# Performance work log

Measured on AMD Instinct MI355X. Metric: run time of the kernel, lower is better.

The kernel has to match this reference:

```python
import jax, jax.numpy as jnp
import numpy as np

EMBED = 1024
B, S = 4, 2048


def setup_inputs() -> dict:
    key = jax.random.key(0)
    ks = jax.random.split(key, 10)
    scale = 1.0 / np.sqrt(EMBED)
    return {
        "query": jax.random.normal(ks[0], (B, S, EMBED), jnp.float32),
        "key": jax.random.normal(ks[1], (B, S, EMBED), jnp.float32),
        "value": jax.random.normal(ks[2], (B, S, EMBED), jnp.float32),
        "attn_mask": jnp.zeros((B, S, S), jnp.float32),
        "Wq": jax.random.normal(ks[3], (EMBED, EMBED), jnp.float32) * scale,
        "bq": jnp.zeros((EMBED,), jnp.float32),
        "Wk": jax.random.normal(ks[4], (EMBED, EMBED), jnp.float32) * scale,
        "bk": jnp.zeros((EMBED,), jnp.float32),
        "Wv": jax.random.normal(ks[5], (EMBED, EMBED), jnp.float32) * scale,
        "bv": jnp.zeros((EMBED,), jnp.float32),
    }


def reference(query, key, value, attn_mask, Wq, bq, Wk, bk, Wv, bv):
    # Linear projections (torch Linear: x @ W.T + b)
    q = jnp.einsum("bse,fe->bsf", query, Wq) + bq
    k = jnp.einsum("bse,fe->bsf", key, Wk) + bk
    v = jnp.einsum("bse,fe->bsf", value, Wv) + bv
    # Scaled dot-product attention; NOTE: scale is sqrt(embed_size) (full dim),
    # matching the original module exactly (num_heads is unused there).
    inv_scale = 1.0 / jnp.sqrt(jnp.asarray(q.shape[-1], q.dtype))
    qk = jnp.einsum("bqe,bke->bqk", q, k) * inv_scale + attn_mask
    attn = jax.nn.softmax(qk, axis=-1)
    # dropout_p = 0.0 (eval-mode identity)
    return jnp.einsum("bqk,bke->bqe", attn, v)
```

## Files before the change

### kernel.cpp

```cpp
#include <hip/hip_runtime.h>
#include <stdint.h>


typedef __attribute__((ext_vector_type(8))) short s8v;
typedef __attribute__((ext_vector_type(4))) float f32x4;
typedef __attribute__((ext_vector_type(4))) unsigned u32x4;

__device__ __forceinline__ unsigned short f2b(float f) {
  union { float f; unsigned u; } c; c.f = f;
  unsigned r = c.u + 0x7fffu + ((c.u >> 16) & 1u);
  return (unsigned short)(r >> 16);
}

__device__ __forceinline__ void gload_lds16(const void* gsrc, void* ldst) {
  __builtin_amdgcn_global_load_lds(
      (__attribute__((address_space(1))) unsigned int*)(uintptr_t)gsrc,
      (__attribute__((address_space(3))) unsigned int*)(unsigned)(uintptr_t)ldst,
      16, 0, 0);
}

template <int N> __device__ __forceinline__ void waitvm() {
  if constexpr (N == 4)      asm volatile("s_waitcnt vmcnt(4)" ::: "memory");
  else if constexpr (N == 3) asm volatile("s_waitcnt vmcnt(3)" ::: "memory");
  else                       asm volatile("s_waitcnt vmcnt(0)" ::: "memory");
}

struct JobF {
  const float* A; const float* B; unsigned short* C; const float* bias;
  long sAb, sBb, sCb;
  int lda, ldb, ldc, tilesN, tilesMN, bmode;
};

__global__ __launch_bounds__(512, 1) void gemmF(JobF j0, JobF j1, JobF j2,
                                                int b0, int b1) {
  constexpr int ASLOT = 256 * 64;
  constexpr int SLOT = 2 * ASLOT;
  constexpr int NT = 32;
  __shared__ __align__(16) char lds[4 * SLOT];

  const int nwg = gridDim.x;
  const int hw = blockIdx.x;
  int g = (hw & 7) * (nwg >> 3) + (hw >> 3);
  const JobF J = (g < b0) ? j0 : (g < b1) ? j1 : j2;
  g -= (g < b0) ? 0 : (g < b1) ? b0 : b1;

  const int batch = g / J.tilesMN;
  const int tt = g - batch * J.tilesMN;
  const int tm = tt / J.tilesN, tn = tt - tm * J.tilesN;
  const int brow = tm << 8, bcol = tn << 8;

  const int tid = threadIdx.x, lane = tid & 63, w = tid >> 6;
  const int wm = w >> 2, wn = w & 3;
  const int fr = lane & 15, fq = lane >> 4;

  const float* Ab = J.A + (long)batch * J.sAb;
  const float* Bb = J.B + (long)batch * J.sBb;

  const float* gsrcF[4];
  int ldsdst[4];
#pragma unroll
  for (int i = 0; i < 4; i++) {
    const int c = w + i * 8;
    const bool isA = (c < 16);
    const int cc = isA ? c : c - 16;
    const int roff = cc * 1024 + lane * 16;
    const int L = roff ^ (((roff >> 7) & 7) << 4);
    const int row = L >> 6, elem = (L & 63) >> 1;
    gsrcF[i] = (isA ? (Ab + (long)(brow + row) * J.lda)
                    : (Bb + (long)(bcol + row) * J.ldb)) + elem;
    ldsdst[i] = (isA ? 0 : ASLOT) + cc * 1024 + lane * 16;
  }

  int offA[8], offB[4];
#pragma unroll
  for (int mi = 0; mi < 8; mi++) {
    const int oa = (wm * 128 + mi * 16 + fr) * 64 + fq * 16;
    offA[mi] = oa ^ (((oa >> 7) & 7) << 4);
  }
#pragma unroll
  for (int ni = 0; ni < 4; ni++) {
    const int ob = (wn * 64 + ni * 16 + fr) * 64 + fq * 16;
    offB[ni] = ASLOT + (ob ^ (((ob >> 7) & 7) << 4));
  }

  f32x4 acc[8][4];
#pragma unroll
  for (int mi = 0; mi < 8; mi++)
#pragma unroll
    for (int ni = 0; ni < 4; ni++) acc[mi][ni] = (f32x4){0.f, 0.f, 0.f, 0.f};

  f32x4 sLo[4], sHi[4];

#define ISSUE(kt) { \
  _Pragma("unroll") \
  for (int i_ = 0; i_ < 4; i_++) { \
    const float* p_ = gsrcF[i_] + (long)(kt) * 32; \
    sLo[i_] = *(const f32x4*)p_; sHi[i_] = *(const f32x4*)(p_ + 4); } }

#define CVTWRITE(kt) { \
  char* const sb_ = lds + ((kt) & 3) * SLOT; \
  _Pragma("unroll") \
  for (int i_ = 0; i_ < 4; i_++) { \
    unsigned o0_, o1_, o2_, o3_; \
    asm("v_cvt_pk_bf16_f32 %0, %1, %2" : "=v"(o0_) : "v"(sLo[i_][0]), "v"(sLo[i_][1])); \
    asm("v_cvt_pk_bf16_f32 %0, %1, %2" : "=v"(o1_) : "v"(sLo[i_][2]), "v"(sLo[i_][3])); \
    asm("v_cvt_pk_bf16_f32 %0, %1, %2" : "=v"(o2_) : "v"(sHi[i_][0]), "v"(sHi[i_][1])); \
    asm("v_cvt_pk_bf16_f32 %0, %1, %2" : "=v"(o3_) : "v"(sHi[i_][2]), "v"(sHi[i_][3])); \
    *(u32x4*)(sb_ + ldsdst[i_]) = (u32x4){o0_, o1_, o2_, o3_}; } }

#define MFMA_BODY(t) { \
  const char* sb_ = lds + ((t) & 3) * SLOT; \
  s8v bf_[4], af_[4]; \
  _Pragma("unroll") \
  for (int ni_ = 0; ni_ < 4; ni_++) bf_[ni_] = *(const s8v*)(sb_ + offB[ni_]); \
  _Pragma("unroll") \
  for (int mi_ = 0; mi_ < 4; mi_++) af_[mi_] = *(const s8v*)(sb_ + offA[mi_]); \
  __builtin_amdgcn_s_setprio(1); \
  _Pragma("unroll") \
  for (int mi_ = 0; mi_ < 4; mi_++) \
    _Pragma("unroll") \
    for (int ni_ = 0; ni_ < 4; ni_++) \
      acc[mi_][ni_] = __builtin_amdgcn_mfma_f32_16x16x32_bf16( \
          af_[mi_], bf_[ni_], acc[mi_][ni_], 0, 0, 0); \
  __builtin_amdgcn_s_setprio(0); \
  _Pragma("unroll") \
  for (int mi_ = 0; mi_ < 4; mi_++) af_[mi_] = *(const s8v*)(sb_ + offA[4 + mi_]); \
  __builtin_amdgcn_s_setprio(1); \
  _Pragma("unroll") \
  for (int mi_ = 0; mi_ < 4; mi_++) \
    _Pragma("unroll") \
    for (int ni_ = 0; ni_ < 4; ni_++) \
      acc[4 + mi_][ni_] = __builtin_amdgcn_mfma_f32_16x16x32_bf16( \
          af_[mi_], bf_[ni_], acc[4 + mi_][ni_], 0, 0, 0); \
  __builtin_amdgcn_s_setprio(0); }

#define ENDBAR() { \
  asm volatile("s_waitcnt lgkmcnt(0)" ::: "memory"); \
  __builtin_amdgcn_s_barrier(); }

  ISSUE(0);
  CVTWRITE(0);
  ISSUE(1);
  ENDBAR();

  for (int t = 0; t < NT; ++t) {
    MFMA_BODY(t);
    if (t + 1 < NT) {
      CVTWRITE(t + 1);
      if (t + 2 < NT) ISSUE(t + 2);
      ENDBAR();
    }
  }

  const long cB = (long)batch * J.sCb;
#pragma unroll
  for (int mi = 0; mi < 8; mi++) {
    const int rbase = brow + wm * 128 + mi * 16 + fq * 4;
#pragma unroll
    for (int ni = 0; ni < 4; ni++) {
      const int col = bcol + wn * 64 + ni * 16 + fr;
      const float bc = (J.bmode == 1) ? J.bias[col] : 0.f;
#pragma unroll
      for (int r = 0; r < 4; r++) {
        const int row = rbase + r;
        float v = acc[mi][ni][r] + ((J.bmode == 2) ? J.bias[row] : bc);
        J.C[cB + (long)row * J.ldc + col] = f2b(v);
      }
    }
  }
#undef ISSUE
#undef CVTWRITE
#undef MFMA_BODY
#undef ENDBAR
}

struct Job {
  const unsigned short* A; const unsigned short* B; void* C;
  const float* bias; const float* mask; float* sRow;
  long sAb, sBb, sCb, sMb;
  int lda, ldb, ldc, ldM;
  int K, tilesN, tilesMN;
  float scale; int bmode;
};

template <int NFRAG, int MODE>
__global__ __launch_bounds__(512, 2) void gemmJ(Job j0, Job j1, Job j2,
                                                int b0, int b1) {
  constexpr int BN = NFRAG * 64;
  constexpr int ASLOT = 256 * 64;
  constexpr int BSLOT = BN * 64;
  constexpr int SLOT = ASLOT + BSLOT;
  constexpr int CH = SLOT / 1024;
  constexpr int GPW = CH / 8;
  static_assert(4 * SLOT <= 160 * 1024, "LDS budget");
  __shared__ __align__(16) char lds[4 * SLOT];

  const int nwg = gridDim.x;
  const int hw = blockIdx.x;
  int g = (hw & 7) * (nwg >> 3) + (hw >> 3);
  const Job J = (g < b0) ? j0 : (g < b1) ? j1 : j2;
  g -= (g < b0) ? 0 : (g < b1) ? b0 : b1;

  const int batch = g / J.tilesMN;
  const int tt = g - batch * J.tilesMN;
  const int tm = tt / J.tilesN, tn = tt - tm * J.tilesN;
  const int brow = tm << 8, bcol = tn * BN;

  const int tid = threadIdx.x;
  const int lane = tid & 63, w = tid >> 6;
  const int wm = w >> 2, wn = w & 3;
  const int fr = lane & 15, fq = lane >> 4;

  const unsigned short* Ab = J.A + (long)batch * J.sAb;
  const unsigned short* Bb = J.B + (long)batch * J.sBb;

  const unsigned short* gsrc[GPW];
  int ldsdst[GPW];
#pragma unroll
  for (int i = 0; i < GPW; i++) {
    const int c = w + i * 8;
    const bool isA = (c < 16);
    const int cc = isA ? c : c - 16;
    const int roff = cc * 1024 + lane * 16;
    const int L = roff ^ (((roff >> 7) & 7) << 4);
    const int row = L >> 6, colb = L & 63;
    gsrc[i] = (isA ? (Ab + (long)(brow + row) * J.lda)
                   : (Bb + (long)(bcol + row) * J.ldb)) + (colb >> 1);
    ldsdst[i] = (isA ? 0 : ASLOT) + cc * 1024;
  }

  int offA[8], offB[NFRAG];
#pragma unroll
  for (int mi = 0; mi < 8; mi++) {
    const int oa = (wm * 128 + mi * 16 + fr) * 64 + fq * 16;
    offA[mi] = oa ^ (((oa >> 7) & 7) << 4);
  }
#pragma unroll
  for (int ni = 0; ni < NFRAG; ni++) {
    const int ob = (wn * (NFRAG * 16) + ni * 16 + fr) * 64 + fq * 16;
    offB[ni] = ASLOT + (ob ^ (((ob >> 7) & 7) << 4));
  }

  f32x4 acc[8][NFRAG];
#pragma unroll
  for (int mi = 0; mi < 8; mi++)
#pragma unroll
    for (int ni = 0; ni < NFRAG; ni++) acc[mi][ni] = (f32x4){0.f, 0.f, 0.f, 0.f};

  const int NT = J.K >> 5;

#define STAGE(kt) { \
  char* const sb_ = lds + ((kt) & 3) * SLOT; \
  _Pragma("unroll") \
  for (int i_ = 0; i_ < GPW; i_++) \
    gload_lds16(gsrc[i_] + (long)(kt) * 32, sb_ + ldsdst[i_]); }

  STAGE(0);
  STAGE(1);
  waitvm<GPW>();
  __builtin_amdgcn_s_barrier();

  for (int t = 0; t < NT; ++t) {
    const char* sb = lds + (t & 3) * SLOT;
    if (t + 2 < NT) STAGE(t + 2);

    s8v bf[NFRAG], af[4];
#pragma unroll
    for (int ni = 0; ni < NFRAG; ni++) bf[ni] = *(const s8v*)(sb + offB[ni]);
#pragma unroll
    for (int mi = 0; mi < 4; mi++) af[mi] = *(const s8v*)(sb + offA[mi]);
    __builtin_amdgcn_s_setprio(1);
#pragma unroll
    for (int mi = 0; mi < 4; mi++)
#pragma unroll
      for (int ni = 0; ni < NFRAG; ni++)
        acc[mi][ni] = __builtin_amdgcn_mfma_f32_16x16x32_bf16(
            af[mi], bf[ni], acc[mi][ni], 0, 0, 0);
    __builtin_amdgcn_s_setprio(0);
#pragma unroll
    for (int mi = 0; mi < 4; mi++) af[mi] = *(const s8v*)(sb + offA[4 + mi]);
    __builtin_amdgcn_s_setprio(1);
#pragma unroll
    for (int mi = 0; mi < 4; mi++)
#pragma unroll
      for (int ni = 0; ni < NFRAG; ni++)
        acc[4 + mi][ni] = __builtin_amdgcn_mfma_f32_16x16x32_bf16(
            af[mi], bf[ni], acc[4 + mi][ni], 0, 0, 0);
    __builtin_amdgcn_s_setprio(0);

    if (t + 1 < NT) {
      if (t + 2 < NT) waitvm<GPW>();
      else            waitvm<0>();
      __builtin_amdgcn_s_barrier();
    }
  }

  unsigned short* Cb = (unsigned short*)J.C;
  float* Cf = (float*)J.C;
  const long cB = (long)batch * J.sCb;
  const float* maskB = (MODE == 1) ? (J.mask + (long)batch * J.sMb) : nullptr;
  float* sB = J.sRow + batch * 2048;

#pragma unroll
  for (int mi = 0; mi < 8; mi++) {
    const int rbase = brow + wm * 128 + mi * 16 + fq * 4;

    if constexpr (MODE == 1) {
      if (J.bmode != 0) {
#pragma unroll
        for (int ni = 0; ni < NFRAG; ni++) {
          const int col = bcol + wn * (NFRAG * 16) + ni * 16 + fr;
          const float bc = (J.bmode == 1) ? J.bias[col] : 0.f;
#pragma unroll
          for (int r = 0; r < 4; r++) {
            const int row = rbase + r;
            float v = acc[mi][ni][r] + ((J.bmode == 2) ? J.bias[row] : bc);
            Cb[cB + (long)row * J.ldc + col] = f2b(v);
          }
        }
      } else {
        float rs[4] = {0.f, 0.f, 0.f, 0.f};
#pragma unroll
        for (int ni = 0; ni < NFRAG; ni++) {
          const int col = bcol + wn * (NFRAG * 16) + ni * 16 + fr;
#pragma unroll
          for (int r = 0; r < 4; r++) {
            const int row = rbase + r;
            float v = acc[mi][ni][r] * J.scale + maskB[(long)row * J.ldM + col];
            v = __expf(v);
            Cb[cB + (long)row * J.ldc + col] = f2b(v);
            rs[r] += v;
          }
        }
#pragma unroll
        for (int off = 1; off < 16; off <<= 1) {
#pragma unroll
          for (int r = 0; r < 4; r++) rs[r] += __shfl_xor(rs[r], off, 64);
        }
        if (fr == 0) {
#pragma unroll
          for (int r = 0; r < 4; r++) atomicAdd(&sB[rbase + r], rs[r]);
        }
      }
    } else {
      float inv[4];
#pragma unroll
      for (int r = 0; r < 4; r++) inv[r] = 1.0f / sB[rbase + r];
#pragma unroll
      for (int ni = 0; ni < NFRAG; ni++) {
        const int col = bcol + wn * (NFRAG * 16) + ni * 16 + fr;
#pragma unroll
        for (int r = 0; r < 4; r++) {
          const int row = rbase + r;
          Cf[cB + (long)row * J.ldc + col] = acc[mi][ni][r] * inv[r];
        }
      }
    }
  }
#undef STAGE
}

__global__ __launch_bounds__(256) void cvtW(
    const float* v, unsigned short* xv,
    const float* Wv, unsigned short* Wvb, float* sz) {
  int bid = blockIdx.x;
  if (bid >= 896) {
    for (int i = (bid - 896) * 256 + threadIdx.x; i < 8192; i += 2048)
      sz[i] = 0.f;
    return;
  }
  const float* src; unsigned short* dst; long n8; int lb, nb;
  if (bid < 768) { src = v;  dst = xv;  n8 = 1048576; lb = bid;       nb = 768; }
  else           { src = Wv; dst = Wvb; n8 = 131072;  lb = bid - 768; nb = 128; }
  const long stride = (long)nb * 256;
  for (long i = (long)lb * 256 + threadIdx.x; i < n8; i += stride) {
    const float* p = src + i * 8;
    f32x4 va = *(const f32x4*)p;
    f32x4 vb = *(const f32x4*)(p + 4);
    s8v o;
    o[0] = (short)f2b(va[0]); o[1] = (short)f2b(va[1]);
    o[2] = (short)f2b(va[2]); o[3] = (short)f2b(va[3]);
    o[4] = (short)f2b(vb[0]); o[5] = (short)f2b(vb[1]);
    o[6] = (short)f2b(vb[2]); o[7] = (short)f2b(vb[3]);
    *(s8v*)(dst + i * 8) = o;
  }
}

extern "C" void kernel_launch(void* const* d_in, const int* in_sizes, int n_in,
                              void* d_out, int out_size, void* d_ws, size_t ws_size,
                              hipStream_t stream) {
  const float* q    = (const float*)d_in[0];
  const float* k    = (const float*)d_in[1];
  const float* v    = (const float*)d_in[2];
  const float* mask = (const float*)d_in[3];
  const float* Wq   = (const float*)d_in[4];
  const float* bq   = (const float*)d_in[5];
  const float* Wk   = (const float*)d_in[6];
  const float* bk   = (const float*)d_in[7];
  const float* Wv   = (const float*)d_in[8];
  const float* bv   = (const float*)d_in[9];
  float* out = (float*)d_out;

  const size_t MB = 1ull << 20;
  if (ws_size < 134 * MB) return;
  char* ws = (char*)d_ws;
  unsigned short* qb  = (unsigned short*)(ws + 0 * MB);
  unsigned short* kb  = (unsigned short*)(ws + 16 * MB);
  unsigned short* vT  = (unsigned short*)(ws + 32 * MB);
  float*          sRw = (float*)(ws + 48 * MB);
  unsigned short* Sb  = (unsigned short*)(ws + 80 * MB);
  unsigned short* xv  = (unsigned short*)(ws + 112 * MB);
  unsigned short* Wvb = (unsigned short*)(ws + 132 * MB);

  cvtW<<<904, 256, 0, stream>>>(v, xv, Wv, Wvb, sRw);

  JobF fq = { q, Wq, qb, bq, 0, 0, 0, 1024, 1024, 1024, 4, 128, 1 };
  JobF fk = { k, Wk, kb, bk, 0, 0, 0, 1024, 1024, 1024, 4, 128, 1 };
  gemmF<<<256, 512, 0, stream>>>(fq, fk, fk, 128, 256);

  Job js = { qb, kb, (void*)Sb, nullptr, mask, sRw,
             2048L * 1024, 2048L * 1024, 2048L * 2048, 2048L * 2048,
             1024, 1024, 2048, 2048, 1024, 8, 64, 0.03125f, 0 };
  Job jv = { Wvb, xv, (void*)vT, bv, nullptr, sRw,
             0, 2048L * 1024, 1024L * 2048, 0,
             1024, 1024, 2048, 0, 1024, 8, 32, 1.0f, 2 };
  gemmJ<4, 1><<<384, 512, 0, stream>>>(js, js, jv, 256, 256);

  Job jp = { Sb, vT, (void*)out, nullptr, nullptr, sRw,
             2048L * 2048, 1024L * 2048, 2048L * 1024, 0,
             2048, 2048, 1024, 0, 2048, 8, 64, 1.0f, 0 };
  gemmJ<2, 2><<<256, 512, 0, stream>>>(jp, jp, jp, 256, 256);
}
```

Before: 216.1 us.

## Replace QK^T/V-projection GEMM with 1024-thread 16-wave kernel using 256x256 tiles

Adds gemmJ16, a 1024-thread (16-wave) workgroup kernel computing 256x256 output tiles with a 4-slot LDS ring and a prefetch distance of two stages. It replaces the 512-thread gemmJ<4,1> launch for the fused QK^T+exp and V-projection jobs, and the MODE==1 epilogue is removed from the templated kernel. The aim is more waves per tile to hide latency and a smaller per-wave accumulator footprint. The trade-off is one workgroup per CU and a shallower prefetch pipeline.

```diff
diff --git a/kernel.cpp b/kernel.cpp
--- a/kernel.cpp
+++ b/kernel.cpp
@@ -22,6 +22,7 @@
 template <int N> __device__ __forceinline__ void waitvm() {
   if constexpr (N == 4)      asm volatile("s_waitcnt vmcnt(4)" ::: "memory");
   else if constexpr (N == 3) asm volatile("s_waitcnt vmcnt(3)" ::: "memory");
+  else if constexpr (N == 2) asm volatile("s_waitcnt vmcnt(2)" ::: "memory");
   else                       asm volatile("s_waitcnt vmcnt(0)" ::: "memory");
 }
 
@@ -183,6 +184,150 @@
   float scale; int bmode;
 };
 
+__global__ __launch_bounds__(1024, 1) void gemmJ16(Job j0, Job j1, Job j2,
+                                                   int b0, int b1) {
+  constexpr int ASLOT = 256 * 64;
+  constexpr int SLOT = 2 * ASLOT;
+  __shared__ __align__(16) char lds[4 * SLOT];
+
+  const int nwg = gridDim.x;
+  const int hw = blockIdx.x;
+  int g = (hw & 7) * (nwg >> 3) + (hw >> 3);
+  const Job J = (g < b0) ? j0 : (g < b1) ? j1 : j2;
+  g -= (g < b0) ? 0 : (g < b1) ? b0 : b1;
+
+  const int batch = g / J.tilesMN;
+  const int tt = g - batch * J.tilesMN;
+  const int tm = tt / J.tilesN, tn = tt - tm * J.tilesN;
+  const int brow = tm << 8, bcol = tn << 8;
+
+  const int tid = threadIdx.x;
+  const int lane = tid & 63, w = tid >> 6;
+  const int wm = w >> 2, wn = w & 3;
+  const int fr = lane & 15, fq = lane >> 4;
+
+  const unsigned short* Ab = J.A + (long)batch * J.sAb;
+  const unsigned short* Bb = J.B + (long)batch * J.sBb;
+
+  const unsigned short* gsrc[2];
+  int ldsdst[2];
+#pragma unroll
+  for (int i = 0; i < 2; i++) {
+    const int c = w + i * 16;
+    const bool isA = (c < 16);
+    const int cc = isA ? c : c - 16;
+    const int roff = cc * 1024 + lane * 16;
+    const int L = roff ^ (((roff >> 7) & 7) << 4);
+    const int row = L >> 6, colb = L & 63;
+    gsrc[i] = (isA ? (Ab + (long)(brow + row) * J.lda)
+                   : (Bb + (long)(bcol + row) * J.ldb)) + (colb >> 1);
+    ldsdst[i] = (isA ? 0 : ASLOT) + cc * 1024;
+  }
+
+  int offA[4], offB[4];
+#pragma unroll
+  for (int mi = 0; mi < 4; mi++) {
+    const int oa = (wm * 64 + mi * 16 + fr) * 64 + fq * 16;
+    offA[mi] = oa ^ (((oa >> 7) & 7) << 4);
+  }
+#pragma unroll
+  for (int ni = 0; ni < 4; ni++) {
+    const int ob = (wn * 64 + ni * 16 + fr) * 64 + fq * 16;
+    offB[ni] = ASLOT + (ob ^ (((ob >> 7) & 7) << 4));
+  }
+
+  f32x4 acc[4][4];
+#pragma unroll
+  for (int mi = 0; mi < 4; mi++)
+#pragma unroll
+    for (int ni = 0; ni < 4; ni++) acc[mi][ni] = (f32x4){0.f, 0.f, 0.f, 0.f};
+
+  const int NT = J.K >> 5;
+
+#define STAGE16(kt) { \
+  char* const sb_ = lds + ((kt) & 3) * SLOT; \
+  gload_lds16(gsrc[0] + (long)(kt) * 32, sb_ + ldsdst[0]); \
+  gload_lds16(gsrc[1] + (long)(kt) * 32, sb_ + ldsdst[1]); }
+
+  STAGE16(0);
+  STAGE16(1);
+  waitvm<2>();
+  __builtin_amdgcn_s_barrier();
+
+  for (int t = 0; t < NT; ++t) {
+    const char* sb = lds + (t & 3) * SLOT;
+    if (t + 2 < NT) STAGE16(t + 2);
+
+    s8v bf[4], af[4];
+#pragma unroll
+    for (int ni = 0; ni < 4; ni++) bf[ni] = *(const s8v*)(sb + offB[ni]);
+#pragma unroll
+    for (int mi = 0; mi < 4; mi++) af[mi] = *(const s8v*)(sb + offA[mi]);
+    __builtin_amdgcn_s_setprio(1);
+#pragma unroll
+    for (int mi = 0; mi < 4; mi++)
+#pragma unroll
+      for (int ni = 0; ni < 4; ni++)
+        acc[mi][ni] = __builtin_amdgcn_mfma_f32_16x16x32_bf16(
+            af[mi], bf[ni], acc[mi][ni], 0, 0, 0);
+    __builtin_amdgcn_s_setprio(0);
+
+    if (t + 1 < NT) {
+      if (t + 2 < NT) waitvm<2>();
+      else            waitvm<0>();
+      __builtin_amdgcn_s_barrier();
+    }
+  }
+
+  unsigned short* Cb = (unsigned short*)J.C;
+  const long cB = (long)batch * J.sCb;
+  const float* maskB = J.mask + (long)batch * J.sMb;
+  float* sB = J.sRow + batch * 2048;
+
+#pragma unroll
+  for (int mi = 0; mi < 4; mi++) {
+    const int rbase = brow + wm * 64 + mi * 16 + fq * 4;
+
+    if (J.bmode != 0) {
+#pragma unroll
+      for (int ni = 0; ni < 4; ni++) {
+        const int col = bcol + wn * 64 + ni * 16 + fr;
+        const float bc = (J.bmode == 1) ? J.bias[col] : 0.f;
+#pragma unroll
+        for (int r = 0; r < 4; r++) {
+          const int row = rbase + r;
+          float v = acc[mi][ni][r] + ((J.bmode == 2) ? J.bias[row] : bc);
+          Cb[cB + (long)row * J.ldc + col] = f2b(v);
+        }
+      }
+    } else {
+      float rs[4] = {0.f, 0.f, 0.f, 0.f};
+#pragma unroll
+      for (int ni = 0; ni < 4; ni++) {
+        const int col = bcol + wn * 64 + ni * 16 + fr;
+#pragma unroll
+        for (int r = 0; r < 4; r++) {
+          const int row = rbase + r;
+          float v = acc[mi][ni][r] * J.scale + maskB[(long)row * J.ldM + col];
+          v = __expf(v);
+          Cb[cB + (long)row * J.ldc + col] = f2b(v);
+          rs[r] += v;
+        }
+      }
+#pragma unroll
+      for (int off = 1; off < 16; off <<= 1) {
+#pragma unroll
+        for (int r = 0; r < 4; r++) rs[r] += __shfl_xor(rs[r], off, 64);
+      }
+      if (fr == 0) {
+#pragma unroll
+        for (int r = 0; r < 4; r++) atomicAdd(&sB[rbase + r], rs[r]);
+      }
+    }
+  }
+#undef STAGE16
+}
+
 template <int NFRAG, int MODE>
 __global__ __launch_bounds__(512, 2) void gemmJ(Job j0, Job j1, Job j2,
                                                 int b0, int b1) {
@@ -192,7 +337,6 @@
   constexpr int SLOT = ASLOT + BSLOT;
   constexpr int CH = SLOT / 1024;
   constexpr int GPW = CH / 8;
-  static_assert(4 * SLOT <= 160 * 1024, "LDS budget");
   __shared__ __align__(16) char lds[4 * SLOT];
 
   const int nwg = gridDim.x;
@@ -295,65 +439,23 @@
     }
   }
 
-  unsigned short* Cb = (unsigned short*)J.C;
   float* Cf = (float*)J.C;
   const long cB = (long)batch * J.sCb;
-  const float* maskB = (MODE == 1) ? (J.mask + (long)batch * J.sMb) : nullptr;
   float* sB = J.sRow + batch * 2048;
 
 #pragma unroll
   for (int mi = 0; mi < 8; mi++) {
     const int rbase = brow + wm * 128 + mi * 16 + fq * 4;
-
-    if constexpr (MODE == 1) {
-      if (J.bmode != 0) {
-#pragma unroll
-        for (int ni = 0; ni < NFRAG; ni++) {
-          const int col = bcol + wn * (NFRAG * 16) + ni * 16 + fr;
-          const float bc = (J.bmode == 1) ? J.bias[col] : 0.f;
-#pragma unroll
-          for (int r = 0; r < 4; r++) {
-            const int row = rbase + r;
-            float v = acc[mi][ni][r] + ((J.bmode == 2) ? J.bias[row] : bc);
-            Cb[cB + (long)row * J.ldc + col] = f2b(v);
-          }
-        }
-      } else {
-        float rs[4] = {0.f, 0.f, 0.f, 0.f};
-#pragma unroll
-        for (int ni = 0; ni < NFRAG; ni++) {
-          const int col = bcol + wn * (NFRAG * 16) + ni * 16 + fr;
-#pragma unroll
-          for (int r = 0; r < 4; r++) {
-            const int row = rbase + r;
-            float v = acc[mi][ni][r] * J.scale + maskB[(long)row * J.ldM + col];
-            v = __expf(v);
-            Cb[cB + (long)row * J.ldc + col] = f2b(v);
-            rs[r] += v;
-          }
-        }
-#pragma unroll
-        for (int off = 1; off < 16; off <<= 1) {
-#pragma unroll
-          for (int r = 0; r < 4; r++) rs[r] += __shfl_xor(rs[r], off, 64);
-        }
-        if (fr == 0) {
-#pragma unroll
-          for (int r = 0; r < 4; r++) atomicAdd(&sB[rbase + r], rs[r]);
-        }
-      }
-    } else {
-      float inv[4];
-#pragma unroll
-      for (int r = 0; r < 4; r++) inv[r] = 1.0f / sB[rbase + r];
-#pragma unroll
-      for (int ni = 0; ni < NFRAG; ni++) {
-        const int col = bcol + wn * (NFRAG * 16) + ni * 16 + fr;
-#pragma unroll
-        for (int r = 0; r < 4; r++) {
-          const int row = rbase + r;
-          Cf[cB + (long)row * J.ldc + col] = acc[mi][ni][r] * inv[r];
-        }
+    float inv[4];
+#pragma unroll
+    for (int r = 0; r < 4; r++) inv[r] = 1.0f / sB[rbase + r];
+#pragma unroll
+    for (int ni = 0; ni < NFRAG; ni++) {
+      const int col = bcol + wn * (NFRAG * 16) + ni * 16 + fr;
+#pragma unroll
+      for (int r = 0; r < 4; r++) {
+        const int row = rbase + r;
+        Cf[cB + (long)row * J.ldc + col] = acc[mi][ni][r] * inv[r];
       }
     }
   }
@@ -421,10 +523,10 @@
   Job js = { qb, kb, (void*)Sb, nullptr, mask, sRw,
              2048L * 1024, 2048L * 1024, 2048L * 2048, 2048L * 2048,
              1024, 1024, 2048, 2048, 1024, 8, 64, 0.03125f, 0 };
-  Job jv = { Wvb, xv, (void*)vT, bv, nullptr, sRw,
+  Job jv = { Wvb, xv, (void*)vT, bv, mask, sRw,
              0, 2048L * 1024, 1024L * 2048, 0,
              1024, 1024, 2048, 0, 1024, 8, 32, 1.0f, 2 };
-  gemmJ<4, 1><<<384, 512, 0, stream>>>(js, js, jv, 256, 256);
+  gemmJ16<<<384, 1024, 0, stream>>>(js, js, jv, 256, 256);
 
   Job jp = { Sb, vT, (void*)out, nullptr, nullptr, sRw,
              2048L * 2048, 1024L * 2048, 2048L * 1024, 0,
```

Result: no change. 213.2 us (-1.3%).
